# Optimization experiments

Hardware: AMD Instinct MI355X
Metric: run time of the kernel (lower is better)

## Reference

```python
import jax, jax.numpy as jnp
import numpy as np

H = 128; L = 3; ODIM = 400; SCALE = 30.0

def gather_nodes(h, E_idx):
    # h: [B,N,C], E_idx: [B,N,K] -> [B,N,K,C]
    B, N, K = E_idx.shape
    C = h.shape[-1]
    idx = jnp.broadcast_to(E_idx.reshape(B, N * K, 1), (B, N * K, C))
    return jnp.take_along_axis(h, idx, axis=1).reshape(B, N, K, C)

def layer_norm(x, eps=1e-5):
    mu = jnp.mean(x, axis=-1, keepdims=True)
    var = jnp.mean((x - mu) ** 2, axis=-1, keepdims=True)
    return (x - mu) / jnp.sqrt(var + eps)

def merge_dups(h_E, inv_mapping):
    # h_E: [B,N,K,C]; inv_mapping: [B,N*K]
    B, N, K, C = h_E.shape
    flat = h_E.reshape(B, N * K, C)
    idx = jnp.broadcast_to(inv_mapping[:, :, None], (B, N * K, C))
    return jnp.take_along_axis(flat, idx, axis=1).reshape(B, N, K, C)

def setup_inputs() -> dict:
    key = jax.random.key(0)
    ks = jax.random.split(key, 40)
    B, N, K = 2, 1024, 30
    d = {}
    d['h_V0'] = jax.random.normal(ks[0], (B, N, H), jnp.float32)
    d['h_E0'] = jax.random.normal(ks[1], (B, N, K, H), jnp.float32)
    d['E_idx'] = jax.random.randint(ks[2], (B, N, K), 0, N, jnp.int32)
    d['inv_mapping'] = jax.random.randint(ks[3], (B, N * K), 0, N * K, jnp.int32)
    d['x_mask'] = jnp.ones((B, N), jnp.float32)
    s = 0.05
    d['Wv_w'] = jax.random.normal(ks[4], (H, H)) * s; d['Wv_b'] = jnp.zeros((H,))
    d['We_w'] = jax.random.normal(ks[5], (H, H)) * s; d['We_b'] = jnp.zeros((H,))
    # node MPNN layers: message MLP (3h->h->h->h) + dense FFN (h->4h->h), stacked [L,...]
    d['nW1'] = jax.random.normal(ks[6], (L, 3 * H, H)) * s; d['nb1'] = jnp.zeros((L, H))
    d['nW2'] = jax.random.normal(ks[7], (L, H, H)) * s;     d['nb2'] = jnp.zeros((L, H))
    d['nW3'] = jax.random.normal(ks[8], (L, H, H)) * s;     d['nb3'] = jnp.zeros((L, H))
    d['nWd1'] = jax.random.normal(ks[9], (L, H, 4 * H)) * s; d['nbd1'] = jnp.zeros((L, 4 * H))
    d['nWd2'] = jax.random.normal(ks[10], (L, 4 * H, H)) * s; d['nbd2'] = jnp.zeros((L, H))
    # edge MPNN layers
    d['eW1'] = jax.random.normal(ks[11], (L, 3 * H, H)) * s; d['eb1'] = jnp.zeros((L, H))
    d['eW2'] = jax.random.normal(ks[12], (L, H, H)) * s;     d['eb2'] = jnp.zeros((L, H))
    d['eW3'] = jax.random.normal(ks[13], (L, H, H)) * s;     d['eb3'] = jnp.zeros((L, H))
    d['eWd1'] = jax.random.normal(ks[14], (L, H, 4 * H)) * s; d['ebd1'] = jnp.zeros((L, 4 * H))
    d['eWd2'] = jax.random.normal(ks[15], (L, 4 * H, H)) * s; d['ebd2'] = jnp.zeros((L, H))
    d['Wout_w'] = jax.random.normal(ks[16], (H, ODIM)) * s; d['Wout_b'] = jnp.zeros((ODIM,))
    return d

def reference(h_V0, h_E0, E_idx, inv_mapping, x_mask,
              Wv_w, Wv_b, We_w, We_b,
              nW1, nb1, nW2, nb2, nW3, nb3, nWd1, nbd1, nWd2, nbd2,
              eW1, eb1, eW2, eb2, eW3, eb3, eWd1, ebd1, eWd2, ebd2,
              Wout_w, Wout_b):
    B, N, K = E_idx.shape
    h_V = h_V0 @ Wv_w + Wv_b                      # W_v embedding
    h_E = h_E0 @ We_w + We_b                      # W_e embedding
    mask_attend = gather_nodes(x_mask[..., None], E_idx)[..., 0] * x_mask[..., None]  # [B,N,K]
    for l in range(L):
        # ---- node update (NodeMPNNLayer) ----
        h_nb = gather_nodes(h_V, E_idx)                           # [B,N,K,H]
        h_i = jnp.broadcast_to(h_V[:, :, None, :], h_nb.shape)
        h_EV = jnp.concatenate([h_i, h_nb, h_E], axis=-1)         # [B,N,K,3H]
        m = jax.nn.relu(h_EV @ nW1[l] + nb1[l])
        m = jax.nn.relu(m @ nW2[l] + nb2[l])
        m = m @ nW3[l] + nb3[l]
        m = m * mask_attend[..., None]
        dh = jnp.sum(m, axis=-2) / SCALE
        h_V = layer_norm(h_V + dh)
        dh = jax.nn.relu(h_V @ nWd1[l] + nbd1[l]) @ nWd2[l] + nbd2[l]
        h_V = layer_norm(h_V + dh)
        h_V = h_V * x_mask[..., None]
        # ---- edge update (EdgeMPNNLayer) ----
        h_j = gather_nodes(h_V, E_idx)
        h_i = jnp.broadcast_to(h_V[:, :, None, :], h_j.shape)
        h_EV = jnp.concatenate([h_i, h_E, h_j], axis=-1)          # [B,N,K,3H]
        m = jax.nn.relu(h_EV @ eW1[l] + eb1[l])
        m = jax.nn.relu(m @ eW2[l] + eb2[l])
        m = m @ eW3[l] + eb3[l]
        h_E = layer_norm(h_E + m)
        dh = jax.nn.relu(h_E @ eWd1[l] + ebd1[l]) @ eWd2[l] + ebd2[l]
        h_E = layer_norm(h_E + dh)
        h_E = h_E * mask_attend[..., None]
    etab = h_E @ Wout_w + Wout_b                                  # [B,N,K,400]
    etab = merge_dups(etab, inv_mapping)
    return etab
```

## Files before the change

kernel.cpp:

```cpp
#include <hip/hip_runtime.h>
#include <hip/hip_bf16.h>
#include <stdint.h>


typedef __bf16 bf16_t;
typedef __attribute__((ext_vector_type(8))) __bf16 bf16x8;
typedef __attribute__((ext_vector_type(4))) float f32x4;

#define B_    2
#define N_    1024
#define KN    30
#define H_    128
#define L_    3
#define ODIM_ 400
#define NK    (N_ * KN)
#define RT    (B_ * N_ * KN)
#define BN_   (B_ * N_)

#define EPI_PLAIN 0
#define EPI_RELU  1
#define EPI_F32   2
#define EPI_ADDUG 3
#define EPI_LN    4
#define EPI_OUT   5

__device__ __forceinline__ float wred(float v) {
#pragma unroll
  for (int off = 32; off > 0; off >>= 1) v += __shfl_xor(v, off, 64);
  return v;
}

__device__ __forceinline__ void gld16(const bf16_t* g, bf16_t* l) {
  __builtin_amdgcn_global_load_lds(
      (__attribute__((address_space(1))) void*)(g),
      (__attribute__((address_space(3))) void*)(l), 16, 0, 0);
}

__device__ __forceinline__ void mm64(const bf16_t* __restrict__ Ah,
                                     const bf16_t* __restrict__ Bh,
                                     int wm, int wn, int fm, int q, int fx,
                                     f32x4 (&acc)[4][4])
{
#pragma unroll
  for (int h = 0; h < 2; ++h) {
    bf16x8 af[4], bfv[4];
#pragma unroll
    for (int mi = 0; mi < 4; ++mi)
      af[mi] = *reinterpret_cast<const bf16x8*>(
          &Ah[(wm * 64 + mi * 16 + fm) * 64 + ((((h << 2) | q) ^ fx) << 3)]);
#pragma unroll
    for (int ni = 0; ni < 4; ++ni)
      bfv[ni] = *reinterpret_cast<const bf16x8*>(
          &Bh[(wn * 64 + ni * 16 + fm) * 64 + ((((h << 2) | q) ^ fx) << 3)]);
#pragma unroll
    for (int mi = 0; mi < 4; ++mi)
#pragma unroll
      for (int ni = 0; ni < 4; ++ni)
        acc[mi][ni] = __builtin_amdgcn_mfma_f32_16x16x32_bf16(
            af[mi], bfv[ni], acc[mi][ni], 0, 0, 0);
  }
}

struct GCArgs {
  const bf16_t* Ain;
  const bf16_t* W1; int koff1; int ldw1;
  const bf16_t* W2; const bf16_t* b2;
  const bf16_t* W3; const bf16_t* b3;
  const float* U; const float* G; const int* E;
  const bf16_t* resid;
  bf16_t* out3;
  const bf16_t* Wd1; const bf16_t* bd1;
  const bf16_t* Wd2; const bf16_t* bd2;
  const float* mvec;
  bf16_t* outF;
};

template<int MODE>
__global__ __launch_bounds__(256, 2) void gc(GCArgs a)
{
  __shared__ __align__(16) bf16_t bufA[2][8192];
  __shared__ __align__(16) bf16_t bufB[2][8192];
  __shared__ __align__(16) bf16_t Ws[8192];
  float* lnS  = (float*)Ws;
  float* lnS2 = lnS + 256;

  const int tid = threadIdx.x;
  const int w = tid >> 6, l = tid & 63;
  const int wm = w & 1, wn = w >> 1;
  const int row0 = blockIdx.x * 128;
  const int lr = l >> 3;
  const int kg8 = ((l & 7) ^ lr) << 3;
  const int fm = l & 15, q = l >> 4, fx = fm & 7;
  const int r4 = w * 32 + lr;

  {
    bf16_t* dst = (MODE == 2) ? bufB[0] : bufA[0];
    const bf16_t* gb = a.Ain + (size_t)(row0 + r4) * 128 + kg8;
#pragma unroll
    for (int kt = 0; kt < 2; ++kt)
#pragma unroll
      for (int s = 0; s < 4; ++s)
        gld16(gb + (size_t)s * 8 * 128 + kt * 64,
              dst + kt * 8192 + w * 2048 + s * 512);
  }

  auto do_gemm = [&](const bf16_t* SRC, const bf16_t* W, int koff, int ldw,
                     f32x4 (&acc)[4][4]) {
#pragma unroll
    for (int kt = 0; kt < 2; ++kt) {
      __syncthreads();
      const bf16_t* gb = W + (size_t)r4 * ldw + koff + kt * 64 + kg8;
#pragma unroll
      for (int s = 0; s < 4; ++s)
        gld16(gb + (size_t)s * 8 * ldw, &Ws[w * 2048 + s * 512]);
      __syncthreads();
      mm64(SRC + kt * 8192, Ws, wm, wn, fm, q, fx, acc);
    }
  };

  auto wb = [&](f32x4 (&acc)[4][4], bf16_t* dst) {
#pragma unroll
    for (int mi = 0; mi < 4; ++mi)
#pragma unroll
      for (int rr = 0; rr < 4; ++rr) {
        int row = wm * 64 + mi * 16 + q * 4 + rr;
#pragma unroll
        for (int ni = 0; ni < 4; ++ni) {
          int cl = ni * 16 + fm;
          dst[wn * 8192 + row * 64 +
              ((((cl >> 3) ^ (row & 7)) << 3) | (cl & 7))] =
              (bf16_t)acc[mi][ni][rr];
        }
      }
  };

  if constexpr (MODE <= 1) {
    f32x4 acc1[4][4] = {};
    do_gemm(bufA[0], a.W1, a.koff1, a.ldw1, acc1);
#pragma unroll
    for (int mi = 0; mi < 4; ++mi)
#pragma unroll
      for (int rr = 0; rr < 4; ++rr) {
        int rg = row0 + wm * 64 + mi * 16 + q * 4 + rr;
        const float* Ur = a.U + (size_t)(rg / KN) * 128;
        const float* Gr = a.G + (size_t)((rg / NK) * N_ + a.E[rg]) * 128;
#pragma unroll
        for (int ni = 0; ni < 4; ++ni) {
          int col = wn * 64 + ni * 16 + fm;
          acc1[mi][ni][rr] = fmaxf(acc1[mi][ni][rr] + Ur[col] + Gr[col], 0.f);
        }
      }
    wb(acc1, bufB[0]);

    f32x4 acc2[4][4] = {};
    do_gemm(bufB[0], a.W2, 0, 128, acc2);
#pragma unroll
    for (int mi = 0; mi < 4; ++mi)
#pragma unroll
      for (int rr = 0; rr < 4; ++rr)
#pragma unroll
        for (int ni = 0; ni < 4; ++ni) {
          int col = wn * 64 + ni * 16 + fm;
          acc2[mi][ni][rr] = fmaxf(acc2[mi][ni][rr] + (float)a.b2[col], 0.f);
        }
    wb(acc2, bufA[0]);

    f32x4 acc3[4][4] = {};
    do_gemm(bufA[0], a.W3, 0, 128, acc3);

    if constexpr (MODE == 0) {
#pragma unroll
      for (int mi = 0; mi < 4; ++mi)
#pragma unroll
        for (int rr = 0; rr < 4; ++rr) {
          size_t rg = (size_t)(row0 + wm * 64 + mi * 16 + q * 4 + rr);
#pragma unroll
          for (int ni = 0; ni < 4; ++ni) {
            int col = wn * 64 + ni * 16 + fm;
            a.out3[rg * 128 + col] =
                (bf16_t)(acc3[mi][ni][rr] + (float)a.b3[col]);
          }
        }
      return;
    } else {
      __syncthreads();
#pragma unroll
      for (int mi = 0; mi < 4; ++mi)
#pragma unroll
        for (int rr = 0; rr < 4; ++rr) {
          int lrow = wm * 64 + mi * 16 + q * 4 + rr;
          size_t rg = (size_t)(row0 + lrow);
          float s = 0.f, s2 = 0.f;
#pragma unroll
          for (int ni = 0; ni < 4; ++ni) {
            int col = wn * 64 + ni * 16 + fm;
            float v = acc3[mi][ni][rr] + (float)a.b3[col]
                      + (float)a.resid[rg * 128 + col];
            acc3[mi][ni][rr] = v;
            s += v; s2 += v * v;
          }
#pragma unroll
          for (int d = 1; d < 16; d <<= 1) {
            s += __shfl_xor(s, d, 64); s2 += __shfl_xor(s2, d, 64);
          }
          if (fm == (mi * 4 + rr)) { lnS[wn * 128 + lrow] = s;
                                     lnS2[wn * 128 + lrow] = s2; }
        }
      __syncthreads();
#pragma unroll
      for (int mi = 0; mi < 4; ++mi)
#pragma unroll
        for (int rr = 0; rr < 4; ++rr) {
          int lrow = wm * 64 + mi * 16 + q * 4 + rr;
          float st = lnS[lrow] + lnS[128 + lrow];
          float st2 = lnS2[lrow] + lnS2[128 + lrow];
          float mu = st * (1.f / 128.f);
          float var = fmaxf(st2 * (1.f / 128.f) - mu * mu, 0.f);
          float rstd = rsqrtf(var + 1e-5f);
#pragma unroll
          for (int ni = 0; ni < 4; ++ni) {
            int cl = ni * 16 + fm;
            bufB[wn][lrow * 64 +
                ((((cl >> 3) ^ (lrow & 7)) << 3) | (cl & 7))] =
                (bf16_t)((acc3[mi][ni][rr] - mu) * rstd);
          }
        }
    }
  }

  {
    f32x4 accF[4][4] = {};
#pragma unroll 1
    for (int c = 0; c < 4; ++c) {
      f32x4 accH[4][4] = {};
      do_gemm(bufB[0], a.Wd1 + (size_t)c * 128 * 128, 0, 128, accH);
#pragma unroll
      for (int mi = 0; mi < 4; ++mi)
#pragma unroll
        for (int rr = 0; rr < 4; ++rr)
#pragma unroll
          for (int ni = 0; ni < 4; ++ni) {
            int col = wn * 64 + ni * 16 + fm;
            accH[mi][ni][rr] =
                fmaxf(accH[mi][ni][rr] + (float)a.bd1[c * 128 + col], 0.f);
          }
      wb(accH, bufA[0]);
      do_gemm(bufA[0], a.Wd2, c * 128, 512, accF);
    }

    __syncthreads();
#pragma unroll
    for (int mi = 0; mi < 4; ++mi)
#pragma unroll
      for (int rr = 0; rr < 4; ++rr) {
        int lrow = wm * 64 + mi * 16 + q * 4 + rr;
        float s = 0.f, s2 = 0.f;
#pragma unroll
        for (int ni = 0; ni < 4; ++ni) {
          int cl = ni * 16 + fm;
          float xv = (float)bufB[wn][lrow * 64 +
              ((((cl >> 3) ^ (lrow & 7)) << 3) | (cl & 7))];
          float v = accF[mi][ni][rr] + (float)a.bd2[wn * 64 + cl] + xv;
          accF[mi][ni][rr] = v;
          s += v; s2 += v * v;
        }
#pragma unroll
        for (int d = 1; d < 16; d <<= 1) {
          s += __shfl_xor(s, d, 64); s2 += __shfl_xor(s2, d, 64);
        }
        if (fm == (mi * 4 + rr)) { lnS[wn * 128 + lrow] = s;
                                   lnS2[wn * 128 + lrow] = s2; }
      }
    __syncthreads();
#pragma unroll
    for (int mi = 0; mi < 4; ++mi)
#pragma unroll
      for (int rr = 0; rr < 4; ++rr) {
        int lrow = wm * 64 + mi * 16 + q * 4 + rr;
        size_t rg = (size_t)(row0 + lrow);
        float st = lnS[lrow] + lnS[128 + lrow];
        float st2 = lnS2[lrow] + lnS2[128 + lrow];
        float mu = st * (1.f / 128.f);
        float var = fmaxf(st2 * (1.f / 128.f) - mu * mu, 0.f);
        float rstd = rsqrtf(var + 1e-5f);
        float mk = a.mvec[rg];
#pragma unroll
        for (int ni = 0; ni < 4; ++ni) {
          int col = wn * 64 + ni * 16 + fm;
          a.outF[rg * 128 + col] =
              (bf16_t)((accF[mi][ni][rr] - mu) * rstd * mk);
        }
      }
  }
}

__global__ __launch_bounds__(256) void gk(
    const bf16_t* __restrict__ A, int lda,
    const bf16_t* __restrict__ Bt, int ldb, int koff,
    const bf16_t* __restrict__ bias,
    int N, int K, int epi,
    bf16_t* __restrict__ C,
    float* __restrict__ Cf, float* __restrict__ Cf1, int koff1,
    const float* __restrict__ U, const float* __restrict__ G,
    const int* __restrict__ E_idx,
    bf16_t* __restrict__ resid, const float* __restrict__ mvec, int row0g,
    const int* __restrict__ inv, const int* __restrict__ flag,
    void* __restrict__ outp)
{
  __shared__ __align__(16) bf16_t As[128 * 64];
  __shared__ __align__(16) bf16_t Bs[128 * 64];
  __shared__ float lnS[2][128];
  __shared__ float lnS2[2][128];

  float* CfD = Cf;
  if (epi == EPI_F32 && blockIdx.z == 1) { koff = koff1; bias = nullptr; CfD = Cf1; }

  const int tid = threadIdx.x;
  const int w = tid >> 6, l = tid & 63;
  const int wm = w & 1, wn = w >> 1;
  const int row0 = blockIdx.y * 128;
  const int col0 = blockIdx.x * 128;
  const int lr = l >> 3;
  const int kg8 = ((l & 7) ^ lr) << 3;

  const bf16_t* ap[4];
  const bf16_t* bp[4];
#pragma unroll
  for (int s = 0; s < 4; ++s) {
    int rA = row0 + w * 32 + s * 8 + lr;
    const bf16_t* abase;
    if (epi == EPI_OUT) {
      int bb = rA / NK;
      abase = A + (size_t)(bb * NK + inv[rA]) * lda;
    } else {
      abase = A + (size_t)rA * lda;
    }
    ap[s] = abase + kg8;
    int rB = col0 + w * 32 + s * 8 + lr;
    if (rB >= N) rB = N - 1;
    bp[s] = Bt + (size_t)rB * ldb + koff + kg8;
  }

  const int fm = l & 15, q = l >> 4, fx = fm & 7;
  f32x4 acc[4][4] = {};

  for (int kt = 0; kt < K; kt += 64) {
    __syncthreads();
#pragma unroll
    for (int s = 0; s < 4; ++s)
      gld16(ap[s] + kt, &As[w * 2048 + s * 512]);
#pragma unroll
    for (int s = 0; s < 4; ++s)
      gld16(bp[s] + kt, &Bs[w * 2048 + s * 512]);
    __syncthreads();
#pragma unroll
    for (int h = 0; h < 2; ++h) {
      bf16x8 af[4], bfv[4];
#pragma unroll
      for (int mi = 0; mi < 4; ++mi)
        af[mi] = *reinterpret_cast<const bf16x8*>(
            &As[(wm * 64 + mi * 16 + fm) * 64 + ((((h << 2) | q) ^ fx) << 3)]);
#pragma unroll
      for (int ni = 0; ni < 4; ++ni)
        bfv[ni] = *reinterpret_cast<const bf16x8*>(
            &Bs[(wn * 64 + ni * 16 + fm) * 64 + ((((h << 2) | q) ^ fx) << 3)]);
#pragma unroll
      for (int mi = 0; mi < 4; ++mi)
#pragma unroll
        for (int ni = 0; ni < 4; ++ni)
          acc[mi][ni] = __builtin_amdgcn_mfma_f32_16x16x32_bf16(
              af[mi], bfv[ni], acc[mi][ni], 0, 0, 0);
    }
  }

  if (epi <= EPI_F32) {
#pragma unroll
    for (int ni = 0; ni < 4; ++ni) {
      int col = col0 + wn * 64 + ni * 16 + fm;
      if (col >= N) continue;
      float bv = bias ? (float)bias[col] : 0.f;
#pragma unroll
      for (int mi = 0; mi < 4; ++mi)
#pragma unroll
        for (int rr = 0; rr < 4; ++rr) {
          size_t rg = (size_t)(row0g + row0 + wm * 64 + mi * 16 + q * 4 + rr);
          float v = acc[mi][ni][rr] + bv;
          if (epi == EPI_RELU) v = fmaxf(v, 0.f);
          if (epi == EPI_F32) CfD[rg * N + col] = v;
          else                C[rg * N + col] = (bf16_t)v;
        }
    }
  } else if (epi == EPI_LN) {
#pragma unroll
    for (int mi = 0; mi < 4; ++mi)
#pragma unroll
      for (int rr = 0; rr < 4; ++rr) {
        int lrow = wm * 64 + mi * 16 + q * 4 + rr;
        size_t rg = (size_t)(row0g + row0 + lrow);
        float s = 0.f, s2 = 0.f;
#pragma unroll
        for (int ni = 0; ni < 4; ++ni) {
          int col = wn * 64 + ni * 16 + fm;
          float v = acc[mi][ni][rr] + (bias ? (float)bias[col] : 0.f)
                    + (float)resid[rg * 128 + col];
          acc[mi][ni][rr] = v;
          s += v; s2 += v * v;
        }
#pragma unroll
        for (int d = 1; d < 16; d <<= 1) {
          s += __shfl_xor(s, d, 64); s2 += __shfl_xor(s2, d, 64);
        }
        if (fm == (mi * 4 + rr)) { lnS[wn][lrow] = s; lnS2[wn][lrow] = s2; }
      }
    __syncthreads();
#pragma unroll
    for (int mi = 0; mi < 4; ++mi)
#pragma unroll
      for (int rr = 0; rr < 4; ++rr) {
        int lrow = wm * 64 + mi * 16 + q * 4 + rr;
        size_t rg = (size_t)(row0g + row0 + lrow);
        float st = lnS[0][lrow] + lnS[1][lrow];
        float st2 = lnS2[0][lrow] + lnS2[1][lrow];
        float mu = st * (1.f / 128.f);
        float var = fmaxf(st2 * (1.f / 128.f) - mu * mu, 0.f);
        float rstd = rsqrtf(var + 1e-5f);
        float mk = mvec ? mvec[rg] : 1.f;
#pragma unroll
        for (int ni = 0; ni < 4; ++ni) {
          int col = wn * 64 + ni * 16 + fm;
          resid[rg * 128 + col] = (bf16_t)((acc[mi][ni][rr] - mu) * rstd * mk);
        }
      }
  } else if (epi == EPI_OUT) {
    const int fl = *flag;
#pragma unroll
    for (int ni = 0; ni < 4; ++ni) {
      int col = col0 + wn * 64 + ni * 16 + fm;
      if (col >= ODIM_) continue;
      float bv = bias ? (float)bias[col] : 0.f;
#pragma unroll
      for (int mi = 0; mi < 4; ++mi)
#pragma unroll
        for (int rr = 0; rr < 4; ++rr) {
          size_t rg = (size_t)(row0 + wm * 64 + mi * 16 + q * 4 + rr);
          float v = acc[mi][ni][rr] + bv;
          size_t idx = rg * ODIM_ + col;
          if (fl) ((bf16_t*)outp)[idx] = (bf16_t)v;
          else    ((float*)outp)[idx]  = v;
        }
    }
  }
}

__global__ void flag_kernel(const uint32_t* __restrict__ xm_raw,
                            int* __restrict__ flag)
{
  if (threadIdx.x == 0 && blockIdx.x == 0)
    *flag = (xm_raw[0] == 0x3F803F80u) ? 1 : 0;
}

struct ConvSeg { const void* src; void* dst; int n; int K; int N; };
struct ConvArgs { ConvSeg s[29]; };

__global__ __launch_bounds__(256) void conv_kernel(
    ConvArgs a, int nseg, int total8, const int* __restrict__ flag)
{
  int t = blockIdx.x * 256 + threadIdx.x;
  if (t >= total8) return;
  const int fl = *flag;
  int seg = 0, t8 = t;
  while (seg < nseg - 1 && t8 >= (a.s[seg].n >> 3)) { t8 -= a.s[seg].n >> 3; ++seg; }
  const ConvSeg sg = a.s[seg];
  const int e = t8 << 3;
  float vals[8];
  if (fl) {
    union { uint4 v; bf16_t b[8]; } u;
    u.v = *((const uint4*)sg.src + t8);
#pragma unroll
    for (int j = 0; j < 8; ++j) vals[j] = (float)u.b[j];
  } else {
    const float* sp = (const float*)sg.src + e;
#pragma unroll
    for (int j = 0; j < 8; ++j) vals[j] = sp[j];
  }
  if (sg.N == 0) {
    union { uint4 v; bf16_t b[8]; } o;
#pragma unroll
    for (int j = 0; j < 8; ++j) o.b[j] = (bf16_t)vals[j];
    *((uint4*)sg.dst + t8) = o.v;
  } else {
    const int KN_ = sg.K * sg.N;
    const int lay = e / KN_;
    const int rem = e - lay * KN_;
    const int k = rem / sg.N;
    const int n0 = rem - k * sg.N;
    bf16_t* dp = (bf16_t*)sg.dst + (size_t)lay * KN_ + k;
#pragma unroll
    for (int j = 0; j < 8; ++j)
      dp[(size_t)(n0 + j) * sg.K] = (bf16_t)vals[j];
  }
}

__global__ __launch_bounds__(256) void mask_kernel(
    const bf16_t* __restrict__ xm, const int* __restrict__ E_idx,
    float* __restrict__ ma, float* __restrict__ xmf)
{
  int r = blockIdx.x * 256 + threadIdx.x;
  if (r >= RT) return;
  if (r < BN_) xmf[r] = (float)xm[r];
  int b = r / NK;
  int n = (r / KN) % N_;
  ma[r] = (float)xm[b * N_ + E_idx[r]] * (float)xm[b * N_ + n];
}

__global__ __launch_bounds__(128) void node_agg_ln_kernel(
    const bf16_t* __restrict__ m3, const float* __restrict__ ma,
    bf16_t* __restrict__ hV)
{
  int bn = blockIdx.x;
  int c = threadIdx.x;
  const bf16_t* mrow = m3 + (size_t)bn * (KN * H_) + c;
  const float* mar = ma + (size_t)bn * KN;
  float s = 0.f;
#pragma unroll
  for (int k = 0; k < KN; ++k) s = fmaf((float)mrow[(size_t)k * H_], mar[k], s);
  float v = (float)hV[(size_t)bn * H_ + c] + s * (1.0f / 30.0f);

  __shared__ float red[4];
  float ss = wred(v), s2 = wred(v * v);
  int w = c >> 6, lane = c & 63;
  if (lane == 0) { red[w * 2] = ss; red[w * 2 + 1] = s2; }
  __syncthreads();
  float tot = red[0] + red[2], tot2 = red[1] + red[3];
  float mu = tot * (1.f / 128.f);
  float var = fmaxf(tot2 * (1.f / 128.f) - mu * mu, 0.f);
  float rstd = rsqrtf(var + 1e-5f);
  hV[(size_t)bn * H_ + c] = (bf16_t)((v - mu) * rstd);
}

extern "C" void kernel_launch(void* const* d_in, const int* in_sizes, int n_in,
                              void* d_out, int out_size, void* d_ws, size_t ws_size,
                              hipStream_t stream)
{
  const int* E_idx  = (const int*)d_in[2];
  const int* invmap = (const int*)d_in[3];

  char* ws = (char*)d_ws;
  size_t woff = 0;
  auto walloc = [&](size_t bytes) -> char* {
    char* p = ws + woff; woff += (bytes + 255) & ~(size_t)255; return p;
  };
  int*    flag  = (int*)walloc(4);
  bf16_t* WtOut = (bf16_t*)walloc((size_t)51200 * 2);
  bf16_t* outbc = (bf16_t*)walloc((size_t)400 * 2);
  bf16_t* hE    = (bf16_t*)walloc((size_t)RT * H_ * 2);

  char* ob = (char*)d_out;
  bf16_t* t0 = (bf16_t*)ob;
  bf16_t* t1 = (bf16_t*)(ob + (size_t)RT * H_ * 2);
  size_t ooff = (size_t)RT * H_ * 2 * 2;
  auto oalloc = [&](size_t bytes) -> char* {
    char* p = ob + ooff; ooff += (bytes + 255) & ~(size_t)255; return p;
  };
  bf16_t* WtV  = (bf16_t*)oalloc(16384 * 2);
  bf16_t* bvc  = (bf16_t*)oalloc(128 * 2);
  bf16_t* WtE  = (bf16_t*)oalloc(16384 * 2);
  bf16_t* bec  = (bf16_t*)oalloc(128 * 2);
  bf16_t* Wtn1 = (bf16_t*)oalloc((size_t)147456 * 2);
  bf16_t* nb1c = (bf16_t*)oalloc(384 * 2);
  bf16_t* Wtn2 = (bf16_t*)oalloc((size_t)49152 * 2);
  bf16_t* nb2c = (bf16_t*)oalloc(384 * 2);
  bf16_t* Wtn3 = (bf16_t*)oalloc((size_t)49152 * 2);
  bf16_t* nb3c = (bf16_t*)oalloc(384 * 2);
  bf16_t* Wtnd1 = (bf16_t*)oalloc((size_t)196608 * 2);
  bf16_t* nbd1c = (bf16_t*)oalloc(1536 * 2);
  bf16_t* Wtnd2 = (bf16_t*)oalloc((size_t)196608 * 2);
  bf16_t* nbd2c = (bf16_t*)oalloc(384 * 2);
  bf16_t* Wte1 = (bf16_t*)oalloc((size_t)147456 * 2);
  bf16_t* eb1c = (bf16_t*)oalloc(384 * 2);
  bf16_t* Wte2 = (bf16_t*)oalloc((size_t)49152 * 2);
  bf16_t* eb2c = (bf16_t*)oalloc(384 * 2);
  bf16_t* Wte3 = (bf16_t*)oalloc((size_t)49152 * 2);
  bf16_t* eb3c = (bf16_t*)oalloc(384 * 2);
  bf16_t* Wted1 = (bf16_t*)oalloc((size_t)196608 * 2);
  bf16_t* ebd1c = (bf16_t*)oalloc(1536 * 2);
  bf16_t* Wted2 = (bf16_t*)oalloc((size_t)196608 * 2);
  bf16_t* ebd2c = (bf16_t*)oalloc(384 * 2);
  float*  Ubuf = (float*)oalloc((size_t)BN_ * 128 * 4);
  float*  Gbuf = (float*)oalloc((size_t)BN_ * 128 * 4);
  bf16_t* hV   = (bf16_t*)oalloc((size_t)BN_ * 128 * 2);
  float*  ma   = (float*)oalloc((size_t)RT * 4);
  bf16_t* xm   = (bf16_t*)oalloc((size_t)BN_ * 2);
  float*  xmf  = (float*)oalloc((size_t)BN_ * 4);

  ConvArgs ca;
  struct D { int idx; void* dst; int K; int N; };
  const D dl[29] = {
    {0, t1, 0, 0}, {1, t0, 0, 0}, {4, xm, 0, 0},
    {5, WtV, 128, 128}, {6, bvc, 0, 0}, {7, WtE, 128, 128}, {8, bec, 0, 0},
    {9, Wtn1, 384, 128}, {10, nb1c, 0, 0}, {11, Wtn2, 128, 128}, {12, nb2c, 0, 0},
    {13, Wtn3, 128, 128}, {14, nb3c, 0, 0},
    {15, Wtnd1, 128, 512}, {16, nbd1c, 0, 0}, {17, Wtnd2, 512, 128}, {18, nbd2c, 0, 0},
    {19, Wte1, 384, 128}, {20, eb1c, 0, 0}, {21, Wte2, 128, 128}, {22, eb2c, 0, 0},
    {23, Wte3, 128, 128}, {24, eb3c, 0, 0},
    {25, Wted1, 128, 512}, {26, ebd1c, 0, 0}, {27, Wted2, 512, 128}, {28, ebd2c, 0, 0},
    {29, WtOut, 128, 400}, {30, outbc, 0, 0}
  };
  int total8 = 0;
  for (int i = 0; i < 29; ++i) {
    ca.s[i].src = d_in[dl[i].idx];
    ca.s[i].dst = dl[i].dst;
    ca.s[i].n   = in_sizes[dl[i].idx];
    ca.s[i].K   = dl[i].K;
    ca.s[i].N   = dl[i].N;
    total8 += ca.s[i].n >> 3;
  }

  auto g = [&](dim3 grid, const bf16_t* A, int lda, const bf16_t* Bt, int ldb,
               int koff, const bf16_t* bias, int N, int K, int epi,
               bf16_t* C, float* Cf, float* Cf1, int koff1,
               bf16_t* resid, const float* mvec, int row0g) {
    gk<<<grid, 256, 0, stream>>>(A, lda, Bt, ldb, koff, bias, N, K, epi,
        C, Cf, Cf1, koff1, Ubuf, Gbuf, E_idx, resid, mvec, row0g,
        invmap, flag, d_out);
  };
  const float* NOM = nullptr;

  flag_kernel<<<1, 64, 0, stream>>>((const uint32_t*)d_in[4], flag);
  conv_kernel<<<(total8 + 255) / 256, 256, 0, stream>>>(ca, 29, total8, flag);
  mask_kernel<<<RT / 256, 256, 0, stream>>>(xm, E_idx, ma, xmf);

  g(dim3(1, BN_ / 128), t1, 128, WtV, 128, 0, bvc, 128, 128, EPI_PLAIN,
    hV, nullptr, nullptr, 0, nullptr, NOM, 0);
  g(dim3(1, RT / 128), t0, 128, WtE, 128, 0, bec, 128, 128, EPI_PLAIN,
    hE, nullptr, nullptr, 0, nullptr, NOM, 0);

  for (int l = 0; l < L_; ++l) {
    g(dim3(1, BN_ / 128, 2), hV, 128, Wtn1 + (size_t)l * 49152, 384, 0,
      nb1c + l * 128, 128, 128, EPI_F32,
      nullptr, Ubuf, Gbuf, 128, nullptr, NOM, 0);
    {
      GCArgs na{};
      na.Ain = hE;
      na.W1 = Wtn1 + (size_t)l * 49152; na.koff1 = 256; na.ldw1 = 384;
      na.W2 = Wtn2 + (size_t)l * 16384; na.b2 = nb2c + l * 128;
      na.W3 = Wtn3 + (size_t)l * 16384; na.b3 = nb3c + l * 128;
      na.U = Ubuf; na.G = Gbuf; na.E = E_idx;
      na.out3 = t0;
      gc<0><<<RT / 128, 256, 0, stream>>>(na);
    }
    node_agg_ln_kernel<<<BN_, 128, 0, stream>>>(t0, ma, hV);
    {
      GCArgs nf{};
      nf.Ain = hV;
      nf.Wd1 = Wtnd1 + (size_t)l * 65536; nf.bd1 = nbd1c + l * 512;
      nf.Wd2 = Wtnd2 + (size_t)l * 65536; nf.bd2 = nbd2c + l * 128;
      nf.mvec = xmf; nf.outF = hV;
      gc<2><<<BN_ / 128, 256, 0, stream>>>(nf);
    }
    g(dim3(1, BN_ / 128, 2), hV, 128, Wte1 + (size_t)l * 49152, 384, 0,
      eb1c + l * 128, 128, 128, EPI_F32,
      nullptr, Ubuf, Gbuf, 256, nullptr, NOM, 0);
    {
      GCArgs ea{};
      ea.Ain = hE;
      ea.W1 = Wte1 + (size_t)l * 49152; ea.koff1 = 128; ea.ldw1 = 384;
      ea.W2 = Wte2 + (size_t)l * 16384; ea.b2 = eb2c + l * 128;
      ea.W3 = Wte3 + (size_t)l * 16384; ea.b3 = eb3c + l * 128;
      ea.U = Ubuf; ea.G = Gbuf; ea.E = E_idx;
      ea.resid = hE;
      ea.Wd1 = Wted1 + (size_t)l * 65536; ea.bd1 = ebd1c + l * 512;
      ea.Wd2 = Wted2 + (size_t)l * 65536; ea.bd2 = ebd2c + l * 128;
      ea.mvec = ma; ea.outF = hE;
      gc<1><<<RT / 128, 256, 0, stream>>>(ea);
    }
  }

  g(dim3(4, RT / 128), hE, 128, WtOut, 128, 0, outbc, ODIM_, 128, EPI_OUT,
    nullptr, nullptr, nullptr, 0, nullptr, NOM, 0);
}
```

Before: 676.3 us.

## Prefetch weight tiles via registers, fuse node aggregation and edge U/G projection

Replaces the per-k-tile global_load_lds weight staging, which took two barriers per tile, with a register prefetch of the next weight tile that overlaps the current MFMA step. The node message kernel now does masked K-sum aggregation through LDS atomics and then global float atomics, so the bf16 message tensor is no longer written and reread. The edge U/G projection is folded into the node FFN kernel, dropping a launch. The edge residual is read from the already-staged LDS input instead of global memory. In exchange there is a zero-fill kernel per layer, atomic contention, nondeterministic float summation order and more register pressure.

```diff
diff --git a/kernel.cpp b/kernel.cpp
--- a/kernel.cpp
+++ b/kernel.cpp
@@ -36,6 +36,17 @@
       (__attribute__((address_space(3))) void*)(l), 16, 0, 0);
 }
 
+__device__ __forceinline__ void bar() {
+  __builtin_amdgcn_sched_barrier(0);
+  __builtin_amdgcn_s_barrier();
+  __builtin_amdgcn_sched_barrier(0);
+}
+__device__ __forceinline__ void barL() {
+  asm volatile("s_waitcnt lgkmcnt(0)" ::: "memory");
+  __builtin_amdgcn_s_barrier();
+  __builtin_amdgcn_sched_barrier(0);
+}
+
 __device__ __forceinline__ void mm64(const bf16_t* __restrict__ Ah,
                                      const bf16_t* __restrict__ Bh,
                                      int wm, int wn, int fm, int q, int fx,
@@ -67,12 +78,14 @@
   const bf16_t* W2; const bf16_t* b2;
   const bf16_t* W3; const bf16_t* b3;
   const float* U; const float* G; const int* E;
-  const bf16_t* resid;
-  bf16_t* out3;
+  const float* ma;
+  float* Agg;
   const bf16_t* Wd1; const bf16_t* bd1;
   const bf16_t* Wd2; const bf16_t* bd2;
   const float* mvec;
   bf16_t* outF;
+  const bf16_t* Wug; const bf16_t* bug;
+  float* Uo; float* Go;
 };
 
 template<int MODE>
@@ -83,6 +96,7 @@
   __shared__ __align__(16) bf16_t Ws[8192];
   float* lnS  = (float*)Ws;
   float* lnS2 = lnS + 256;
+  float* aggS = (float*)Ws;
 
   const int tid = threadIdx.x;
   const int w = tid >> 6, l = tid & 63;
@@ -93,29 +107,26 @@
   const int fm = l & 15, q = l >> 4, fx = fm & 7;
   const int r4 = w * 32 + lr;
 
-  {
-    bf16_t* dst = (MODE == 2) ? bufB[0] : bufA[0];
-    const bf16_t* gb = a.Ain + (size_t)(row0 + r4) * 128 + kg8;
-#pragma unroll
-    for (int kt = 0; kt < 2; ++kt)
-#pragma unroll
-      for (int s = 0; s < 4; ++s)
-        gld16(gb + (size_t)s * 8 * 128 + kt * 64,
-              dst + kt * 8192 + w * 2048 + s * 512);
-  }
-
-  auto do_gemm = [&](const bf16_t* SRC, const bf16_t* W, int koff, int ldw,
-                     f32x4 (&acc)[4][4]) {
-#pragma unroll
-    for (int kt = 0; kt < 2; ++kt) {
-      __syncthreads();
-      const bf16_t* gb = W + (size_t)r4 * ldw + koff + kt * 64 + kg8;
-#pragma unroll
-      for (int s = 0; s < 4; ++s)
-        gld16(gb + (size_t)s * 8 * ldw, &Ws[w * 2048 + s * 512]);
-      __syncthreads();
-      mm64(SRC + kt * 8192, Ws, wm, wn, fm, q, fx, acc);
-    }
+  bf16x8 R[4];
+
+  auto wload = [&](const bf16_t* W, int ldw, int koff) {
+    const bf16_t* gb = W + (size_t)r4 * ldw + koff + kg8;
+#pragma unroll
+    for (int s = 0; s < 4; ++s)
+      R[s] = *reinterpret_cast<const bf16x8*>(gb + (size_t)(s * 8) * ldw);
+  };
+
+  auto kt_step = [&](const bf16_t* Wn, int ldwn, int koffn,
+                     const bf16_t* SRC, f32x4 (&acc)[4][4]) {
+    bar();
+#pragma unroll
+    for (int s = 0; s < 4; ++s)
+      *reinterpret_cast<bf16x8*>(&Ws[w * 2048 + s * 512 + l * 8]) = R[s];
+    wload(Wn, ldwn, koffn);
+    asm volatile("s_waitcnt lgkmcnt(0)" ::: "memory");
+    __builtin_amdgcn_s_barrier();
+    __builtin_amdgcn_sched_barrier(0);
+    mm64(SRC, Ws, wm, wn, fm, q, fx, acc);
   };
 
   auto wb = [&](f32x4 (&acc)[4][4], bf16_t* dst) {
@@ -134,9 +145,24 @@
       }
   };
 
+  if constexpr (MODE <= 1) wload(a.W1, a.ldw1, a.koff1);
+  else                     wload(a.Wd1, 128, 0);
+  {
+    bf16_t* dst = (MODE == 2) ? bufB[0] : bufA[0];
+    const bf16_t* gb = a.Ain + (size_t)(row0 + r4) * 128 + kg8;
+#pragma unroll
+    for (int kt = 0; kt < 2; ++kt)
+#pragma unroll
+      for (int s = 0; s < 4; ++s)
+        gld16(gb + (size_t)(s * 8) * 128 + kt * 64,
+              dst + kt * 8192 + w * 2048 + s * 512);
+  }
+  __syncthreads();
+
   if constexpr (MODE <= 1) {
     f32x4 acc1[4][4] = {};
-    do_gemm(bufA[0], a.W1, a.koff1, a.ldw1, acc1);
+    kt_step(a.W1, a.ldw1, a.koff1 + 64, bufA[0], acc1);
+    kt_step(a.W2, 128, 0,               bufA[0] + 8192, acc1);
 #pragma unroll
     for (int mi = 0; mi < 4; ++mi)
 #pragma unroll
@@ -153,7 +179,8 @@
     wb(acc1, bufB[0]);
 
     f32x4 acc2[4][4] = {};
-    do_gemm(bufB[0], a.W2, 0, 128, acc2);
+    kt_step(a.W2, 128, 64, bufB[0], acc2);
+    kt_step(a.W3, 128, 0,  bufB[0] + 8192, acc2);
 #pragma unroll
     for (int mi = 0; mi < 4; ++mi)
 #pragma unroll
@@ -163,39 +190,57 @@
           int col = wn * 64 + ni * 16 + fm;
           acc2[mi][ni][rr] = fmaxf(acc2[mi][ni][rr] + (float)a.b2[col], 0.f);
         }
-    wb(acc2, bufA[0]);
+    bar();
+    wb(acc2, bufB[0]);
 
     f32x4 acc3[4][4] = {};
-    do_gemm(bufA[0], a.W3, 0, 128, acc3);
+    kt_step(a.W3, 128, 64, bufB[0], acc3);
+    if constexpr (MODE == 0)
+      kt_step(a.W3, 128, 64, bufB[0] + 8192, acc3);
+    else
+      kt_step(a.Wd1, 128, 0, bufB[0] + 8192, acc3);
 
     if constexpr (MODE == 0) {
+      bar();
+      for (int i = tid; i < 768; i += 256) aggS[i] = 0.f;
+      barL();
+      const int nb0 = row0 / KN;
 #pragma unroll
       for (int mi = 0; mi < 4; ++mi)
 #pragma unroll
         for (int rr = 0; rr < 4; ++rr) {
-          size_t rg = (size_t)(row0 + wm * 64 + mi * 16 + q * 4 + rr);
+          int rg = row0 + wm * 64 + mi * 16 + q * 4 + rr;
+          float mav = a.ma[rg];
+          int nl = rg / KN - nb0;
 #pragma unroll
           for (int ni = 0; ni < 4; ++ni) {
             int col = wn * 64 + ni * 16 + fm;
-            a.out3[rg * 128 + col] =
-                (bf16_t)(acc3[mi][ni][rr] + (float)a.b3[col]);
+            atomicAdd(&aggS[nl * 128 + col],
+                      (acc3[mi][ni][rr] + (float)a.b3[col]) * mav);
           }
         }
+      barL();
+      const int nbL = (row0 + 127) / KN;
+      for (int i = tid; i < 768; i += 256) {
+        int ng = nb0 + (i >> 7);
+        if (ng <= nbL)
+          atomicAdd(&a.Agg[(size_t)ng * 128 + (i & 127)], aggS[i]);
+      }
       return;
     } else {
-      __syncthreads();
+      bar();
 #pragma unroll
       for (int mi = 0; mi < 4; ++mi)
 #pragma unroll
         for (int rr = 0; rr < 4; ++rr) {
           int lrow = wm * 64 + mi * 16 + q * 4 + rr;
-          size_t rg = (size_t)(row0 + lrow);
           float s = 0.f, s2 = 0.f;
 #pragma unroll
           for (int ni = 0; ni < 4; ++ni) {
-            int col = wn * 64 + ni * 16 + fm;
-            float v = acc3[mi][ni][rr] + (float)a.b3[col]
-                      + (float)a.resid[rg * 128 + col];
+            int cl = ni * 16 + fm;
+            float rv = (float)bufA[wn][lrow * 64 +
+                ((((cl >> 3) ^ (lrow & 7)) << 3) | (cl & 7))];
+            float v = acc3[mi][ni][rr] + (float)a.b3[wn * 64 + cl] + rv;
             acc3[mi][ni][rr] = v;
             s += v; s2 += v * v;
           }
@@ -206,7 +251,7 @@
           if (fm == (mi * 4 + rr)) { lnS[wn * 128 + lrow] = s;
                                      lnS2[wn * 128 + lrow] = s2; }
         }
-      __syncthreads();
+      barL();
 #pragma unroll
       for (int mi = 0; mi < 4; ++mi)
 #pragma unroll
@@ -232,8 +277,10 @@
     f32x4 accF[4][4] = {};
 #pragma unroll 1
     for (int c = 0; c < 4; ++c) {
+      const bf16_t* Wd1c = a.Wd1 + (size_t)c * 16384;
       f32x4 accH[4][4] = {};
-      do_gemm(bufB[0], a.Wd1 + (size_t)c * 128 * 128, 0, 128, accH);
+      kt_step(Wd1c, 128, 64,      bufB[0], accH);
+      kt_step(a.Wd2, 512, c * 128, bufB[0] + 8192, accH);
 #pragma unroll
       for (int mi = 0; mi < 4; ++mi)
 #pragma unroll
@@ -245,10 +292,15 @@
                 fmaxf(accH[mi][ni][rr] + (float)a.bd1[c * 128 + col], 0.f);
           }
       wb(accH, bufA[0]);
-      do_gemm(bufA[0], a.Wd2, c * 128, 512, accF);
-    }
-
-    __syncthreads();
+      kt_step(a.Wd2, 512, c * 128 + 64, bufA[0], accF);
+      const bf16_t* nxt; int nldw, nkoff;
+      if (c < 3)            { nxt = a.Wd1 + (size_t)(c + 1) * 16384; nldw = 128; nkoff = 0; }
+      else if (MODE == 2)   { nxt = a.Wug; nldw = 384; nkoff = 0; }
+      else                  { nxt = a.Wd2; nldw = 512; nkoff = c * 128 + 64; }
+      kt_step(nxt, nldw, nkoff, bufA[0] + 8192, accF);
+    }
+
+    bar();
 #pragma unroll
     for (int mi = 0; mi < 4; ++mi)
 #pragma unroll
@@ -271,7 +323,7 @@
         if (fm == (mi * 4 + rr)) { lnS[wn * 128 + lrow] = s;
                                    lnS2[wn * 128 + lrow] = s2; }
       }
-    __syncthreads();
+    barL();
 #pragma unroll
     for (int mi = 0; mi < 4; ++mi)
 #pragma unroll
@@ -287,10 +339,44 @@
 #pragma unroll
         for (int ni = 0; ni < 4; ++ni) {
           int col = wn * 64 + ni * 16 + fm;
-          a.outF[rg * 128 + col] =
-              (bf16_t)((accF[mi][ni][rr] - mu) * rstd * mk);
+          float ov = (accF[mi][ni][rr] - mu) * rstd * mk;
+          a.outF[rg * 128 + col] = (bf16_t)ov;
+          if constexpr (MODE == 2) accF[mi][ni][rr] = ov;
         }
       }
+
+    if constexpr (MODE == 2) {
+      bar();
+      wb(accF, bufB[0]);
+      f32x4 accU[4][4] = {};
+      kt_step(a.Wug, 384, 64,  bufB[0], accU);
+      kt_step(a.Wug, 384, 256, bufB[0] + 8192, accU);
+#pragma unroll
+      for (int mi = 0; mi < 4; ++mi)
+#pragma unroll
+        for (int rr = 0; rr < 4; ++rr) {
+          size_t rg = (size_t)(row0 + wm * 64 + mi * 16 + q * 4 + rr);
+#pragma unroll
+          for (int ni = 0; ni < 4; ++ni) {
+            int col = wn * 64 + ni * 16 + fm;
+            a.Uo[rg * 128 + col] = accU[mi][ni][rr] + (float)a.bug[col];
+          }
+        }
+      f32x4 accG[4][4] = {};
+      kt_step(a.Wug, 384, 320, bufB[0], accG);
+      kt_step(a.Wug, 384, 320, bufB[0] + 8192, accG);
+#pragma unroll
+      for (int mi = 0; mi < 4; ++mi)
+#pragma unroll
+        for (int rr = 0; rr < 4; ++rr) {
+          size_t rg = (size_t)(row0 + wm * 64 + mi * 16 + q * 4 + rr);
+#pragma unroll
+          for (int ni = 0; ni < 4; ++ni) {
+            int col = wn * 64 + ni * 16 + fm;
+            a.Go[rg * 128 + col] = accG[mi][ni][rr];
+          }
+        }
+    }
   }
 }
 
@@ -513,19 +599,19 @@
   ma[r] = (float)xm[b * N_ + E_idx[r]] * (float)xm[b * N_ + n];
 }
 
-__global__ __launch_bounds__(128) void node_agg_ln_kernel(
-    const bf16_t* __restrict__ m3, const float* __restrict__ ma,
-    bf16_t* __restrict__ hV)
+__global__ __launch_bounds__(256) void zero_kernel(float* __restrict__ p, int n)
+{
+  int i = blockIdx.x * 256 + threadIdx.x;
+  if (i < n) p[i] = 0.f;
+}
+
+__global__ __launch_bounds__(128) void node_ln_kernel(
+    const float* __restrict__ Agg, bf16_t* __restrict__ hV)
 {
   int bn = blockIdx.x;
   int c = threadIdx.x;
-  const bf16_t* mrow = m3 + (size_t)bn * (KN * H_) + c;
-  const float* mar = ma + (size_t)bn * KN;
-  float s = 0.f;
-#pragma unroll
-  for (int k = 0; k < KN; ++k) s = fmaf((float)mrow[(size_t)k * H_], mar[k], s);
-  float v = (float)hV[(size_t)bn * H_ + c] + s * (1.0f / 30.0f);
-
+  float v = (float)hV[(size_t)bn * H_ + c] +
+            Agg[(size_t)bn * H_ + c] * (1.0f / 30.0f);
   __shared__ float red[4];
   float ss = wred(v), s2 = wred(v * v);
   int w = c >> 6, lane = c & 63;
@@ -592,6 +678,7 @@
   float*  ma   = (float*)oalloc((size_t)RT * 4);
   bf16_t* xm   = (bf16_t*)oalloc((size_t)BN_ * 2);
   float*  xmf  = (float*)oalloc((size_t)BN_ * 4);
+  float*  Abuf = (float*)oalloc((size_t)BN_ * 128 * 4);
 
   ConvArgs ca;
   struct D { int idx; void* dst; int K; int N; };
@@ -639,6 +726,7 @@
     g(dim3(1, BN_ / 128, 2), hV, 128, Wtn1 + (size_t)l * 49152, 384, 0,
       nb1c + l * 128, 128, 128, EPI_F32,
       nullptr, Ubuf, Gbuf, 128, nullptr, NOM, 0);
+    zero_kernel<<<(BN_ * 128) / 256, 256, 0, stream>>>(Abuf, BN_ * 128);
     {
       GCArgs na{};
       na.Ain = hE;
@@ -646,21 +734,20 @@
       na.W2 = Wtn2 + (size_t)l * 16384; na.b2 = nb2c + l * 128;
       na.W3 = Wtn3 + (size_t)l * 16384; na.b3 = nb3c + l * 128;
       na.U = Ubuf; na.G = Gbuf; na.E = E_idx;
-      na.out3 = t0;
+      na.ma = ma; na.Agg = Abuf;
       gc<0><<<RT / 128, 256, 0, stream>>>(na);
     }
-    node_agg_ln_kernel<<<BN_, 128, 0, stream>>>(t0, ma, hV);
+    node_ln_kernel<<<BN_, 128, 0, stream>>>(Abuf, hV);
     {
       GCArgs nf{};
       nf.Ain = hV;
       nf.Wd1 = Wtnd1 + (size_t)l * 65536; nf.bd1 = nbd1c + l * 512;
       nf.Wd2 = Wtnd2 + (size_t)l * 65536; nf.bd2 = nbd2c + l * 128;
       nf.mvec = xmf; nf.outF = hV;
+      nf.Wug = Wte1 + (size_t)l * 49152; nf.bug = eb1c + l * 128;
+      nf.Uo = Ubuf; nf.Go = Gbuf;
       gc<2><<<BN_ / 128, 256, 0, stream>>>(nf);
     }
-    g(dim3(1, BN_ / 128, 2), hV, 128, Wte1 + (size_t)l * 49152, 384, 0,
-      eb1c + l * 128, 128, 128, EPI_F32,
-      nullptr, Ubuf, Gbuf, 256, nullptr, NOM, 0);
     {
       GCArgs ea{};
       ea.Ain = hE;
@@ -668,7 +755,6 @@
       ea.W2 = Wte2 + (size_t)l * 16384; ea.b2 = eb2c + l * 128;
       ea.W3 = Wte3 + (size_t)l * 16384; ea.b3 = eb3c + l * 128;
       ea.U = Ubuf; ea.G = Gbuf; ea.E = E_idx;
-      ea.resid = hE;
       ea.Wd1 = Wted1 + (size_t)l * 65536; ea.bd1 = ebd1c + l * 512;
       ea.Wd2 = Wted2 + (size_t)l * 65536; ea.bd2 = ebd2c + l * 128;
       ea.mvec = ma; ea.outF = hE;
```

Result: slower. 782.9 us (+15.8%).
